# Optimization experiments

Measured on AMD Instinct MI355X. Metric: run time of the kernel, lower is better.

Reference implementation:

```python
import jax, jax.numpy as jnp
import numpy as np

LN_EPS = 1e-5

def _layer_norm(x, g, b):
    mu = jnp.mean(x, axis=-1, keepdims=True)
    var = jnp.var(x, axis=-1, keepdims=True)
    return (x - mu) * jax.lax.rsqrt(var + LN_EPS) * g + b

def _mlp(x, W1, b1, g1, beta1, W2, b2):
    h = x @ W1 + b1
    h = _layer_norm(h, g1, beta1)
    h = jax.nn.silu(h)
    return h @ W2 + b2

def setup_inputs() -> dict:
    key = jax.random.key(0)
    ks = jax.random.split(key, 16)
    N, E = 50000, 600000
    node_dim, edge_dim, hidden = 128, 128, 256
    def lin(k, fan_in, fan_out):
        bound = 1.0 / np.sqrt(fan_in)
        kw, kb = jax.random.split(k)
        W = jax.random.uniform(kw, (fan_in, fan_out), jnp.float32, -bound, bound)
        b = jax.random.uniform(kb, (fan_out,), jnp.float32, -bound, bound)
        return W, b
    eW1, eb1 = lin(ks[0], 2 * node_dim + edge_dim, hidden)
    eW2, eb2 = lin(ks[1], hidden, edge_dim)
    nW1, nb1 = lin(ks[2], node_dim + edge_dim, hidden)
    nW2, nb2 = lin(ks[3], hidden, node_dim)
    return {
        "node_features": jax.random.normal(ks[4], (N, node_dim), jnp.float32),
        "edge_features": jax.random.normal(ks[5], (E, edge_dim), jnp.float32),
        "edge_index": jax.random.randint(ks[6], (2, E), 0, N, jnp.int64),
        "eW1": eW1, "eb1": eb1, "eg1": jnp.ones((hidden,), jnp.float32), "ebeta1": jnp.zeros((hidden,), jnp.float32),
        "eW2": eW2, "eb2": eb2,
        "nW1": nW1, "nb1": nb1, "ng1": jnp.ones((hidden,), jnp.float32), "nbeta1": jnp.zeros((hidden,), jnp.float32),
        "nW2": nW2, "nb2": nb2,
    }

def reference(node_features, edge_features, edge_index,
              eW1, eb1, eg1, ebeta1, eW2, eb2,
              nW1, nb1, ng1, nbeta1, nW2, nb2):
    senders = edge_index[0]
    receivers = edge_index[1]
    # gather -> edge MLP (residual)
    edge_input = jnp.concatenate(
        [node_features[senders], node_features[receivers], edge_features], axis=-1)  # [E, 2*nd+ed]
    edge_features = edge_features + _mlp(edge_input, eW1, eb1, eg1, ebeta1, eW2, eb2)
    # scatter-add aggregate over receivers
    n_nodes = node_features.shape[0]
    aggregated = jax.ops.segment_sum(edge_features, receivers, num_segments=n_nodes)
    # node MLP (residual)
    node_input = jnp.concatenate([node_features, aggregated], axis=-1)  # [N, nd+ed]
    node_features = node_features + _mlp(node_input, nW1, nb1, ng1, nbeta1, nW2, nb2)
    return node_features, edge_features
```

## Files before the change

kernel.cpp:

```cpp
#include <hip/hip_runtime.h>

#define N_NODES 50000
#define N_EDGES 600000
#define DIM 128
#define HID 256
#define MR 32

typedef float  f32x4  __attribute__((ext_vector_type(4), aligned(16), may_alias));
typedef float  f32x2  __attribute__((ext_vector_type(2), aligned(8),  may_alias));
typedef __bf16 bf16x8 __attribute__((ext_vector_type(8), aligned(16), may_alias));
typedef int    i32x4  __attribute__((ext_vector_type(4), aligned(16), may_alias));

static __device__ inline f32x4 mfma16x16x32(bf16x8 a, bf16x8 b, f32x4 c) {
    return __builtin_amdgcn_mfma_f32_16x16x32_bf16(a, b, c, 0, 0, 0);
}

static __device__ inline bf16x8 cvt2_bf16(f32x4 a, f32x4 b) {
    bf16x8 o;
    o[0] = (__bf16)a[0]; o[1] = (__bf16)a[1]; o[2] = (__bf16)a[2]; o[3] = (__bf16)a[3];
    o[4] = (__bf16)b[0]; o[5] = (__bf16)b[1]; o[6] = (__bf16)b[2]; o[7] = (__bf16)b[3];
    return o;
}

__global__ void nbf_kernel(const float* __restrict__ node, __bf16* __restrict__ nbf) {
    int idx = blockIdx.x * 256 + threadIdx.x;
    if (idx >= N_NODES * 16) return;
    int row = idx >> 4, c = idx & 15;
    const float* p = node + (size_t)row * DIM + (c << 3);
    f32x4 a = ((const f32x4*)p)[0], b = ((const f32x4*)p)[1];
    *(bf16x8*)(nbf + (size_t)row * DIM + (c << 3)) = cvt2_bf16(a, b);
}

static __device__ inline void pack_one(const float* __restrict__ W,
                                       __bf16* __restrict__ out,
                                       int idx, int Ncols) {
    int lane = idx & 63;
    int tc = idx >> 6;
    int nC = Ncols >> 4;
    int c = tc % nC;
    int t = tc / nC;
    int col = (c << 4) + (lane & 15);
    int k0 = (t << 5) + ((lane >> 4) << 3);
    bf16x8 v;
#pragma unroll
    for (int j = 0; j < 8; ++j) v[j] = (__bf16)W[(k0 + j) * Ncols + col];
    *((bf16x8*)out + idx) = v;
}

__global__ void pack_all_kernel(const float* __restrict__ eW1, const float* __restrict__ eW2,
                                const float* __restrict__ nW1, const float* __restrict__ nW2,
                                __bf16* __restrict__ peW1, __bf16* __restrict__ peW2,
                                __bf16* __restrict__ pnW1, __bf16* __restrict__ pnW2) {
    int idx = blockIdx.x * 256 + threadIdx.x;
    if (idx < 12288)       pack_one(eW1, peW1, idx, 256);
    else if (idx < 16384)  pack_one(eW2, peW2, idx - 12288, 128);
    else if (idx < 24576)  pack_one(nW1, pnW1, idx - 16384, 256);
    else                   pack_one(nW2, pnW2, idx - 24576, 128);
}

__global__ void hist_kernel(const int* __restrict__ eidx, int* __restrict__ counts) {
    int e = blockIdx.x * 256 + threadIdx.x;
    if (e < N_EDGES) {
        int r = eidx[N_EDGES + e];
        r = (r < 0) ? 0 : (r >= N_NODES ? N_NODES - 1 : r);
        atomicAdd(&counts[r], 1);
    }
}

__global__ __launch_bounds__(1024) void scan_kernel(const int* __restrict__ counts,
                                                    int* __restrict__ offsets,
                                                    int* __restrict__ cursor) {
    __shared__ int part[1024];
    const int t = threadIdx.x;
    const int CH = (N_NODES + 1023) / 1024;
    const int base = t * CH;
    int s = 0;
#pragma unroll 1
    for (int i = 0; i < CH; ++i) {
        int idx = base + i;
        if (idx < N_NODES) s += counts[idx];
    }
    part[t] = s;
    __syncthreads();
    for (int d = 1; d < 1024; d <<= 1) {
        int x = (t >= d) ? part[t - d] : 0;
        __syncthreads();
        part[t] += x;
        __syncthreads();
    }
    int run = part[t] - s;
#pragma unroll 1
    for (int i = 0; i < CH; ++i) {
        int idx = base + i;
        if (idx < N_NODES) {
            offsets[idx] = run;
            cursor[idx]  = run;
            run += counts[idx];
        }
    }
    if (t == 1023) offsets[N_NODES] = run;
}

__global__ void scatter_kernel(const int* __restrict__ eidx,
                               int* __restrict__ cursor, int* __restrict__ eids) {
    int e = blockIdx.x * 256 + threadIdx.x;
    if (e < N_EDGES) {
        int r = eidx[N_EDGES + e];
        r = (r < 0) ? 0 : (r >= N_NODES ? N_NODES - 1 : r);
        int pos = atomicAdd(&cursor[r], 1);
        eids[pos] = e;
    }
}

template<int ASTRIDE, int T1>
__device__ inline void mlp_core(char* lds,
                                const bf16x8* __restrict__ pW1,
                                const bf16x8* __restrict__ pW2,
                                const float* __restrict__ b1,
                                const float* __restrict__ g1,
                                const float* __restrict__ be1,
                                f32x4 (&acc2)[2][2]) {
    const int tid = threadIdx.x;
    const int w = tid >> 6;
    const int lane = tid & 63;
    const int l16 = lane & 15;
    const int g = lane >> 4;
    float* stats = (float*)(lds + 32 * ASTRIDE);

    f32x4 acc[2][4];
#pragma unroll
    for (int m = 0; m < 2; ++m)
#pragma unroll
        for (int n = 0; n < 4; ++n) acc[m][n] = (f32x4){0.f, 0.f, 0.f, 0.f};
#pragma unroll
    for (int t = 0; t < T1; ++t) {
        bf16x8 af[2];
#pragma unroll
        for (int m = 0; m < 2; ++m)
            af[m] = *(const bf16x8*)(lds + (m * 16 + l16) * ASTRIDE + t * 64 + g * 16);
        const bf16x8* bp = pW1 + ((t * 16 + 4 * w) << 6) + lane;
#pragma unroll
        for (int n = 0; n < 4; ++n) {
            bf16x8 bf = bp[n << 6];
#pragma unroll
            for (int m = 0; m < 2; ++m)
                acc[m][n] = mfma16x16x32(af[m], bf, acc[m][n]);
        }
    }

    float b1v[4];
#pragma unroll
    for (int n = 0; n < 4; ++n) b1v[n] = b1[64 * w + 16 * n + l16];
#pragma unroll
    for (int m = 0; m < 2; ++m) {
#pragma unroll
        for (int n = 0; n < 4; ++n) acc[m][n] += b1v[n];
        f32x4 s = (acc[m][0] + acc[m][1]) + (acc[m][2] + acc[m][3]);
        f32x4 q = acc[m][0] * acc[m][0];
        q = acc[m][1] * acc[m][1] + q;
        q = acc[m][2] * acc[m][2] + q;
        q = acc[m][3] * acc[m][3] + q;
#pragma unroll
        for (int st = 1; st <= 8; st <<= 1) {
#pragma unroll
            for (int r = 0; r < 4; ++r) {
                s[r] += __shfl_xor(s[r], st);
                q[r] += __shfl_xor(q[r], st);
            }
        }
        if (l16 == 0) {
#pragma unroll
            for (int r = 0; r < 4; ++r) {
                int row = m * 16 + g * 4 + r;
                *(f32x2*)(stats + row * 8 + w * 2) = (f32x2){s[r], q[r]};
            }
        }
    }
    __syncthreads();

    f32x4 mu4[2], rs4[2];
#pragma unroll
    for (int m = 0; m < 2; ++m)
#pragma unroll
        for (int r = 0; r < 4; ++r) {
            int row = m * 16 + g * 4 + r;
            f32x4 a = *(const f32x4*)(stats + row * 8);
            f32x4 b = *(const f32x4*)(stats + row * 8 + 4);
            float S = (a[0] + a[2]) + (b[0] + b[2]);
            float Q = (a[1] + a[3]) + (b[1] + b[3]);
            float mm = S * (1.f / 256.f);
            float vv = fmaxf(Q * (1.f / 256.f) - mm * mm, 0.f);
            mu4[m][r] = mm;
            rs4[m][r] = __builtin_amdgcn_rsqf(vv + 1e-5f);
        }
    float g1v[4], bev[4];
#pragma unroll
    for (int n = 0; n < 4; ++n) {
        g1v[n] = g1[64 * w + 16 * n + l16];
        bev[n] = be1[64 * w + 16 * n + l16];
    }
#pragma unroll
    for (int m = 0; m < 2; ++m)
#pragma unroll
        for (int n = 0; n < 4; ++n) {
            f32x4 y = (acc[m][n] - mu4[m]) * rs4[m];
            y = y * g1v[n] + bev[n];
            int col = 64 * w + 16 * n + l16;
#pragma unroll
            for (int r = 0; r < 4; ++r) {
                float e = __builtin_amdgcn_exp2f(y[r] * -1.44269504f);
                float x = y[r] * __builtin_amdgcn_rcpf(1.f + e);
                int row = m * 16 + g * 4 + r;
                *(__bf16*)(lds + row * 528 + col * 2) = (__bf16)x;
            }
        }
    __syncthreads();

#pragma unroll
    for (int m = 0; m < 2; ++m)
#pragma unroll
        for (int n = 0; n < 2; ++n) acc2[m][n] = (f32x4){0.f, 0.f, 0.f, 0.f};
#pragma unroll
    for (int t = 0; t < 8; ++t) {
        bf16x8 af[2];
#pragma unroll
        for (int m = 0; m < 2; ++m)
            af[m] = *(const bf16x8*)(lds + (m * 16 + l16) * 528 + t * 64 + g * 16);
        const bf16x8* bp = pW2 + ((t * 8 + 2 * w) << 6) + lane;
#pragma unroll
        for (int n = 0; n < 2; ++n) {
            bf16x8 bf = bp[n << 6];
#pragma unroll
            for (int m = 0; m < 2; ++m)
                acc2[m][n] = mfma16x16x32(af[m], bf, acc2[m][n]);
        }
    }
}

__global__ __launch_bounds__(256, 5) void edge_kernel(
    const __bf16* __restrict__ nbf, const float* __restrict__ ef,
    const int* __restrict__ eidx,
    const bf16x8* __restrict__ pW1, const bf16x8* __restrict__ pW2,
    const float* __restrict__ b1, const float* __restrict__ g1,
    const float* __restrict__ be1, const float* __restrict__ b2,
    float* __restrict__ out_edges) {
    __shared__ __align__(16) char lds[MR * 784 + MR * 32];
    const int tid = threadIdx.x;
    const int eb = blockIdx.x * MR;

    {
        int row = tid >> 3, l8 = tid & 7;
        int e = eb + row;
        int snd = eidx[e], rcv = eidx[N_EDGES + e];
        snd = (snd < 0) ? 0 : (snd >= N_NODES ? N_NODES - 1 : snd);
        rcv = (rcv < 0) ? 0 : (rcv >= N_NODES ? N_NODES - 1 : rcv);
        const char* ps = (const char*)(nbf + (size_t)snd * DIM) + (l8 << 5);
        const char* pr = (const char*)(nbf + (size_t)rcv * DIM) + (l8 << 5);
        char* dst = lds + row * 784 + (l8 << 5);
        *(i32x4*)dst         = *(const i32x4*)ps;
        *(i32x4*)(dst + 16)  = *(const i32x4*)(ps + 16);
        *(i32x4*)(dst + 256) = *(const i32x4*)pr;
        *(i32x4*)(dst + 272) = *(const i32x4*)(pr + 16);
        const float* pe = ef + (size_t)e * DIM + (l8 << 4);
        f32x4 a0 = ((const f32x4*)pe)[0], a1 = ((const f32x4*)pe)[1];
        f32x4 a2 = ((const f32x4*)pe)[2], a3 = ((const f32x4*)pe)[3];
        *(bf16x8*)(dst + 512) = cvt2_bf16(a0, a1);
        *(bf16x8*)(dst + 528) = cvt2_bf16(a2, a3);
    }
    __syncthreads();

    f32x4 acc2[2][2];
    mlp_core<784, 12>(lds, pW1, pW2, b1, g1, be1, acc2);

    {
        const int w = tid >> 6, lane = tid & 63;
        const int l16 = lane & 15, g = lane >> 4;
        float b2v[2];
#pragma unroll
        for (int n = 0; n < 2; ++n) b2v[n] = b2[32 * w + 16 * n + l16];
#pragma unroll
        for (int m = 0; m < 2; ++m)
#pragma unroll
            for (int n = 0; n < 2; ++n)
#pragma unroll
                for (int r = 0; r < 4; ++r) {
                    int e = eb + m * 16 + g * 4 + r;
                    int col = 32 * w + 16 * n + l16;
                    size_t off = (size_t)e * DIM + col;
                    out_edges[off] = acc2[m][n][r] + b2v[n] + ef[off];
                }
    }
}

__global__ __launch_bounds__(256, 5) void node_kernel(
    const float* __restrict__ node, const __bf16* __restrict__ nbf,
    const float* __restrict__ out_edges,
    const int* __restrict__ offsets, const int* __restrict__ eids,
    const bf16x8* __restrict__ pW1, const bf16x8* __restrict__ pW2,
    const float* __restrict__ b1, const float* __restrict__ g1,
    const float* __restrict__ be1, const float* __restrict__ b2,
    float* __restrict__ out_nodes) {
    __shared__ __align__(16) char lds[MR * 528 + MR * 32];
    const int tid = threadIdx.x;
    const int nb = blockIdx.x * MR;

    {
        int row = tid >> 3, l8 = tid & 7;
        int n = nb + row;
        int nc = (n > N_NODES - 1) ? N_NODES - 1 : n;
        const char* pn = (const char*)(nbf + (size_t)nc * DIM) + (l8 << 5);
        char* dst = lds + row * 528 + (l8 << 5);
        *(i32x4*)dst        = *(const i32x4*)pn;
        *(i32x4*)(dst + 16) = *(const i32x4*)(pn + 16);
        float a[16];
#pragma unroll
        for (int j = 0; j < 16; ++j) a[j] = 0.f;
        int st = offsets[nc], en = offsets[nc + 1];
        int i = st;
#pragma unroll 1
        for (; i + 2 <= en; i += 2) {
            int e0 = eids[i], e1 = eids[i + 1];
            const float* er0 = out_edges + (size_t)e0 * DIM + (l8 << 4);
            const float* er1 = out_edges + (size_t)e1 * DIM + (l8 << 4);
            f32x4 u0 = ((const f32x4*)er0)[0], u1 = ((const f32x4*)er0)[1];
            f32x4 u2 = ((const f32x4*)er0)[2], u3 = ((const f32x4*)er0)[3];
            f32x4 v0 = ((const f32x4*)er1)[0], v1 = ((const f32x4*)er1)[1];
            f32x4 v2 = ((const f32x4*)er1)[2], v3 = ((const f32x4*)er1)[3];
#pragma unroll
            for (int k = 0; k < 4; ++k) {
                a[0 + k]  += u0[k] + v0[k];
                a[4 + k]  += u1[k] + v1[k];
                a[8 + k]  += u2[k] + v2[k];
                a[12 + k] += u3[k] + v3[k];
            }
        }
        if (i < en) {
            int e0 = eids[i];
            const float* er0 = out_edges + (size_t)e0 * DIM + (l8 << 4);
#pragma unroll
            for (int k = 0; k < 4; ++k) {
                f32x4 v = ((const f32x4*)er0)[k];
                a[k * 4 + 0] += v[0]; a[k * 4 + 1] += v[1];
                a[k * 4 + 2] += v[2]; a[k * 4 + 3] += v[3];
            }
        }
        bf16x8 o0, o1;
#pragma unroll
        for (int j = 0; j < 8; ++j) { o0[j] = (__bf16)a[j]; o1[j] = (__bf16)a[8 + j]; }
        int cbase = 16 + (l8 << 1);
        *(bf16x8*)(lds + row * 528 + (cbase << 4)) = o0;
        *(bf16x8*)(lds + row * 528 + ((cbase + 1) << 4)) = o1;
    }
    __syncthreads();

    f32x4 acc2[2][2];
    mlp_core<528, 8>(lds, pW1, pW2, b1, g1, be1, acc2);

    {
        const int w = tid >> 6, lane = tid & 63;
        const int l16 = lane & 15, g = lane >> 4;
        float b2v[2];
#pragma unroll
        for (int n = 0; n < 2; ++n) b2v[n] = b2[32 * w + 16 * n + l16];
#pragma unroll
        for (int m = 0; m < 2; ++m)
#pragma unroll
            for (int n = 0; n < 2; ++n)
#pragma unroll
                for (int r = 0; r < 4; ++r) {
                    int nd = nb + m * 16 + g * 4 + r;
                    if (nd < N_NODES) {
                        int col = 32 * w + 16 * n + l16;
                        size_t off = (size_t)nd * DIM + col;
                        out_nodes[off] = acc2[m][n][r] + b2v[n] + node[off];
                    }
                }
    }
}

extern "C" void kernel_launch(void* const* d_in, const int* in_sizes, int n_in,
                              void* d_out, int out_size, void* d_ws, size_t ws_size,
                              hipStream_t stream) {
    const float* node  = (const float*)d_in[0];
    const float* ef    = (const float*)d_in[1];
    const int*   eidx  = (const int*)d_in[2];
    const float* eW1   = (const float*)d_in[3];
    const float* eb1   = (const float*)d_in[4];
    const float* eg1   = (const float*)d_in[5];
    const float* ebt1  = (const float*)d_in[6];
    const float* eW2   = (const float*)d_in[7];
    const float* eb2   = (const float*)d_in[8];
    const float* nW1   = (const float*)d_in[9];
    const float* nb1   = (const float*)d_in[10];
    const float* ng1   = (const float*)d_in[11];
    const float* nbt1  = (const float*)d_in[12];
    const float* nW2   = (const float*)d_in[13];
    const float* nb2   = (const float*)d_in[14];

    char* ws = (char*)d_ws;
    int* counts  = (int*)ws;
    int* offsets = counts + 50016;
    int* cursor  = offsets + 50016;
    int* eids    = cursor + 50016;
    char* nbase = (char*)(eids + 600064);
    __bf16* nbf = (__bf16*)(((uintptr_t)nbase + 255) & ~(uintptr_t)255);
    __bf16* peW1 = nbf + (size_t)N_NODES * DIM;
    __bf16* peW2 = peW1 + 384 * 256;
    __bf16* pnW1 = peW2 + 256 * 128;
    __bf16* pnW2 = pnW1 + 256 * 256;

    hipMemsetAsync(counts, 0, 50000 * sizeof(int), stream);
    nbf_kernel<<<(N_NODES * 16 + 255) / 256, 256, 0, stream>>>(node, nbf);
    pack_all_kernel<<<112, 256, 0, stream>>>(eW1, eW2, nW1, nW2, peW1, peW2, pnW1, pnW2);

    hist_kernel<<<(N_EDGES + 255) / 256, 256, 0, stream>>>(eidx, counts);
    scan_kernel<<<1, 1024, 0, stream>>>(counts, offsets, cursor);
    scatter_kernel<<<(N_EDGES + 255) / 256, 256, 0, stream>>>(eidx, cursor, eids);

    float* out_nodes = (float*)d_out;
    float* out_edges = out_nodes + (size_t)N_NODES * DIM;

    edge_kernel<<<N_EDGES / MR, 256, 0, stream>>>(
        nbf, ef, eidx, (const bf16x8*)peW1, (const bf16x8*)peW2,
        eb1, eg1, ebt1, eb2, out_edges);
    node_kernel<<<(N_NODES + MR - 1) / MR, 256, 0, stream>>>(
        node, nbf, out_edges, offsets, eids, (const bf16x8*)pnW1, (const bf16x8*)pnW2,
        nb1, ng1, nbt1, nb2, out_nodes);
}
```

Before: 618.9 us.

## Double MLP row tile to 64 with 8-wave blocks and centralized LayerNorm stats

Raises rows per block from 32 to 64 and launches 512-thread blocks. Each wave now computes 4 row tiles by a narrower column slice, so every weight fragment loaded from global memory feeds twice as many MFMAs, roughly halving weight traffic per row. LayerNorm mean and rstd are now computed once per row by 64 threads and shared through LDS, instead of every lane recomputing them. The cost is a larger LDS footprint per block, which can lower the number of resident blocks per CU, and more accumulator registers per wave.

```diff
diff --git a/kernel.cpp b/kernel.cpp
--- a/kernel.cpp
+++ b/kernel.cpp
@@ -4,7 +4,7 @@
 #define N_EDGES 600000
 #define DIM 128
 #define HID 256
-#define MR 32
+#define MR 64
 
 typedef float  f32x4  __attribute__((ext_vector_type(4), aligned(16), may_alias));
 typedef float  f32x2  __attribute__((ext_vector_type(2), aligned(8),  may_alias));
@@ -113,53 +113,51 @@
 }
 
 template<int ASTRIDE, int T1>
-__device__ inline void mlp_core(char* lds,
-                                const bf16x8* __restrict__ pW1,
-                                const bf16x8* __restrict__ pW2,
-                                const float* __restrict__ b1,
-                                const float* __restrict__ g1,
-                                const float* __restrict__ be1,
-                                f32x4 (&acc2)[2][2]) {
+__device__ inline void mlp_core8(char* lds,
+                                 const bf16x8* __restrict__ pW1,
+                                 const bf16x8* __restrict__ pW2,
+                                 const float* __restrict__ b1,
+                                 const float* __restrict__ g1,
+                                 const float* __restrict__ be1,
+                                 f32x4 (&acc2)[4]) {
     const int tid = threadIdx.x;
     const int w = tid >> 6;
     const int lane = tid & 63;
     const int l16 = lane & 15;
     const int g = lane >> 4;
-    float* stats = (float*)(lds + 32 * ASTRIDE);
-
-    f32x4 acc[2][4];
-#pragma unroll
-    for (int m = 0; m < 2; ++m)
-#pragma unroll
-        for (int n = 0; n < 4; ++n) acc[m][n] = (f32x4){0.f, 0.f, 0.f, 0.f};
+    float* stats = (float*)(lds + 64 * ASTRIDE);
+
+    f32x4 acc[4][2];
+#pragma unroll
+    for (int m = 0; m < 4; ++m)
+#pragma unroll
+        for (int n = 0; n < 2; ++n) acc[m][n] = (f32x4){0.f, 0.f, 0.f, 0.f};
 #pragma unroll
     for (int t = 0; t < T1; ++t) {
-        bf16x8 af[2];
-#pragma unroll
-        for (int m = 0; m < 2; ++m)
+        bf16x8 af[4];
+#pragma unroll
+        for (int m = 0; m < 4; ++m)
             af[m] = *(const bf16x8*)(lds + (m * 16 + l16) * ASTRIDE + t * 64 + g * 16);
-        const bf16x8* bp = pW1 + ((t * 16 + 4 * w) << 6) + lane;
-#pragma unroll
-        for (int n = 0; n < 4; ++n) {
+        const bf16x8* bp = pW1 + ((t * 16 + 2 * w) << 6) + lane;
+#pragma unroll
+        for (int n = 0; n < 2; ++n) {
             bf16x8 bf = bp[n << 6];
 #pragma unroll
-            for (int m = 0; m < 2; ++m)
+            for (int m = 0; m < 4; ++m)
                 acc[m][n] = mfma16x16x32(af[m], bf, acc[m][n]);
         }
     }
 
-    float b1v[4];
-#pragma unroll
-    for (int n = 0; n < 4; ++n) b1v[n] = b1[64 * w + 16 * n + l16];
-#pragma unroll
-    for (int m = 0; m < 2; ++m) {
-#pragma unroll
-        for (int n = 0; n < 4; ++n) acc[m][n] += b1v[n];
-        f32x4 s = (acc[m][0] + acc[m][1]) + (acc[m][2] + acc[m][3]);
+    float b1v[2];
+#pragma unroll
+    for (int n = 0; n < 2; ++n) b1v[n] = b1[32 * w + 16 * n + l16];
+#pragma unroll
+    for (int m = 0; m < 4; ++m) {
+        acc[m][0] += b1v[0];
+        acc[m][1] += b1v[1];
+        f32x4 s = acc[m][0] + acc[m][1];
         f32x4 q = acc[m][0] * acc[m][0];
         q = acc[m][1] * acc[m][1] + q;
-        q = acc[m][2] * acc[m][2] + q;
-        q = acc[m][3] * acc[m][3] + q;
 #pragma unroll
         for (int st = 1; st <= 8; st <<= 1) {
 #pragma unroll
@@ -172,40 +170,46 @@
 #pragma unroll
             for (int r = 0; r < 4; ++r) {
                 int row = m * 16 + g * 4 + r;
-                *(f32x2*)(stats + row * 8 + w * 2) = (f32x2){s[r], q[r]};
-            }
-        }
-    }
-    __syncthreads();
-
-    f32x4 mu4[2], rs4[2];
-#pragma unroll
-    for (int m = 0; m < 2; ++m)
+                *(f32x2*)(stats + row * 16 + w * 2) = (f32x2){s[r], q[r]};
+            }
+        }
+    }
+    __syncthreads();
+
+    if (tid < 64) {
+        const float* sp = stats + tid * 16;
+        f32x4 a = *(const f32x4*)sp;
+        f32x4 b = *(const f32x4*)(sp + 4);
+        f32x4 c = *(const f32x4*)(sp + 8);
+        f32x4 d = *(const f32x4*)(sp + 12);
+        float S = ((a[0] + a[2]) + (b[0] + b[2])) + ((c[0] + c[2]) + (d[0] + d[2]));
+        float Q = ((a[1] + a[3]) + (b[1] + b[3])) + ((c[1] + c[3]) + (d[1] + d[3]));
+        float mm = S * (1.f / 256.f);
+        float vv = fmaxf(Q * (1.f / 256.f) - mm * mm, 0.f);
+        *(f32x2*)(stats + tid * 16) = (f32x2){mm, __builtin_amdgcn_rsqf(vv + 1e-5f)};
+    }
+    __syncthreads();
+
+    float g1v[2], bev[2];
+#pragma unroll
+    for (int n = 0; n < 2; ++n) {
+        g1v[n] = g1[32 * w + 16 * n + l16];
+        bev[n] = be1[32 * w + 16 * n + l16];
+    }
+#pragma unroll
+    for (int m = 0; m < 4; ++m) {
+        f32x4 mu4, rs4;
 #pragma unroll
         for (int r = 0; r < 4; ++r) {
             int row = m * 16 + g * 4 + r;
-            f32x4 a = *(const f32x4*)(stats + row * 8);
-            f32x4 b = *(const f32x4*)(stats + row * 8 + 4);
-            float S = (a[0] + a[2]) + (b[0] + b[2]);
-            float Q = (a[1] + a[3]) + (b[1] + b[3]);
-            float mm = S * (1.f / 256.f);
-            float vv = fmaxf(Q * (1.f / 256.f) - mm * mm, 0.f);
-            mu4[m][r] = mm;
-            rs4[m][r] = __builtin_amdgcn_rsqf(vv + 1e-5f);
-        }
-    float g1v[4], bev[4];
-#pragma unroll
-    for (int n = 0; n < 4; ++n) {
-        g1v[n] = g1[64 * w + 16 * n + l16];
-        bev[n] = be1[64 * w + 16 * n + l16];
-    }
-#pragma unroll
-    for (int m = 0; m < 2; ++m)
-#pragma unroll
-        for (int n = 0; n < 4; ++n) {
-            f32x4 y = (acc[m][n] - mu4[m]) * rs4[m];
+            f32x2 v = *(const f32x2*)(stats + row * 16);
+            mu4[r] = v[0]; rs4[r] = v[1];
+        }
+#pragma unroll
+        for (int n = 0; n < 2; ++n) {
+            f32x4 y = (acc[m][n] - mu4) * rs4;
             y = y * g1v[n] + bev[n];
-            int col = 64 * w + 16 * n + l16;
+            int col = 32 * w + 16 * n + l16;
 #pragma unroll
             for (int r = 0; r < 4; ++r) {
                 float e = __builtin_amdgcn_exp2f(y[r] * -1.44269504f);
@@ -214,37 +218,32 @@
                 *(__bf16*)(lds + row * 528 + col * 2) = (__bf16)x;
             }
         }
-    __syncthreads();
-
-#pragma unroll
-    for (int m = 0; m < 2; ++m)
-#pragma unroll
-        for (int n = 0; n < 2; ++n) acc2[m][n] = (f32x4){0.f, 0.f, 0.f, 0.f};
+    }
+    __syncthreads();
+
+#pragma unroll
+    for (int m = 0; m < 4; ++m) acc2[m] = (f32x4){0.f, 0.f, 0.f, 0.f};
 #pragma unroll
     for (int t = 0; t < 8; ++t) {
-        bf16x8 af[2];
-#pragma unroll
-        for (int m = 0; m < 2; ++m)
+        bf16x8 af[4];
+#pragma unroll
+        for (int m = 0; m < 4; ++m)
             af[m] = *(const bf16x8*)(lds + (m * 16 + l16) * 528 + t * 64 + g * 16);
-        const bf16x8* bp = pW2 + ((t * 8 + 2 * w) << 6) + lane;
-#pragma unroll
-        for (int n = 0; n < 2; ++n) {
-            bf16x8 bf = bp[n << 6];
-#pragma unroll
-            for (int m = 0; m < 2; ++m)
-                acc2[m][n] = mfma16x16x32(af[m], bf, acc2[m][n]);
-        }
-    }
-}
-
-__global__ __launch_bounds__(256, 5) void edge_kernel(
+        bf16x8 bf = pW2[((t * 8 + w) << 6) + lane];
+#pragma unroll
+        for (int m = 0; m < 4; ++m)
+            acc2[m] = mfma16x16x32(af[m], bf, acc2[m]);
+    }
+}
+
+__global__ __launch_bounds__(512, 6) void edge_kernel(
     const __bf16* __restrict__ nbf, const float* __restrict__ ef,
     const int* __restrict__ eidx,
     const bf16x8* __restrict__ pW1, const bf16x8* __restrict__ pW2,
     const float* __restrict__ b1, const float* __restrict__ g1,
     const float* __restrict__ be1, const float* __restrict__ b2,
     float* __restrict__ out_edges) {
-    __shared__ __align__(16) char lds[MR * 784 + MR * 32];
+    __shared__ __align__(16) char lds[MR * 784 + MR * 64];
     const int tid = threadIdx.x;
     const int eb = blockIdx.x * MR;
 
@@ -269,30 +268,26 @@
     }
     __syncthreads();
 
-    f32x4 acc2[2][2];
-    mlp_core<784, 12>(lds, pW1, pW2, b1, g1, be1, acc2);
+    f32x4 acc2[4];
+    mlp_core8<784, 12>(lds, pW1, pW2, b1, g1, be1, acc2);
 
     {
         const int w = tid >> 6, lane = tid & 63;
         const int l16 = lane & 15, g = lane >> 4;
-        float b2v[2];
-#pragma unroll
-        for (int n = 0; n < 2; ++n) b2v[n] = b2[32 * w + 16 * n + l16];
-#pragma unroll
-        for (int m = 0; m < 2; ++m)
-#pragma unroll
-            for (int n = 0; n < 2; ++n)
-#pragma unroll
-                for (int r = 0; r < 4; ++r) {
-                    int e = eb + m * 16 + g * 4 + r;
-                    int col = 32 * w + 16 * n + l16;
-                    size_t off = (size_t)e * DIM + col;
-                    out_edges[off] = acc2[m][n][r] + b2v[n] + ef[off];
-                }
-    }
-}
-
-__global__ __launch_bounds__(256, 5) void node_kernel(
+        const int col = 16 * w + l16;
+        float b2v = b2[col];
+#pragma unroll
+        for (int m = 0; m < 4; ++m)
+#pragma unroll
+            for (int r = 0; r < 4; ++r) {
+                int e = eb + m * 16 + g * 4 + r;
+                size_t off = (size_t)e * DIM + col;
+                out_edges[off] = acc2[m][r] + b2v + ef[off];
+            }
+    }
+}
+
+__global__ __launch_bounds__(512, 6) void node_kernel(
     const float* __restrict__ node, const __bf16* __restrict__ nbf,
     const float* __restrict__ out_edges,
     const int* __restrict__ offsets, const int* __restrict__ eids,
@@ -300,7 +295,7 @@
     const float* __restrict__ b1, const float* __restrict__ g1,
     const float* __restrict__ be1, const float* __restrict__ b2,
     float* __restrict__ out_nodes) {
-    __shared__ __align__(16) char lds[MR * 528 + MR * 32];
+    __shared__ __align__(16) char lds[MR * 528 + MR * 64];
     const int tid = threadIdx.x;
     const int nb = blockIdx.x * MR;
 
@@ -353,28 +348,24 @@
     }
     __syncthreads();
 
-    f32x4 acc2[2][2];
-    mlp_core<528, 8>(lds, pW1, pW2, b1, g1, be1, acc2);
+    f32x4 acc2[4];
+    mlp_core8<528, 8>(lds, pW1, pW2, b1, g1, be1, acc2);
 
     {
         const int w = tid >> 6, lane = tid & 63;
         const int l16 = lane & 15, g = lane >> 4;
-        float b2v[2];
-#pragma unroll
-        for (int n = 0; n < 2; ++n) b2v[n] = b2[32 * w + 16 * n + l16];
-#pragma unroll
-        for (int m = 0; m < 2; ++m)
-#pragma unroll
-            for (int n = 0; n < 2; ++n)
-#pragma unroll
-                for (int r = 0; r < 4; ++r) {
-                    int nd = nb + m * 16 + g * 4 + r;
-                    if (nd < N_NODES) {
-                        int col = 32 * w + 16 * n + l16;
-                        size_t off = (size_t)nd * DIM + col;
-                        out_nodes[off] = acc2[m][n][r] + b2v[n] + node[off];
-                    }
+        const int col = 16 * w + l16;
+        float b2v = b2[col];
+#pragma unroll
+        for (int m = 0; m < 4; ++m)
+#pragma unroll
+            for (int r = 0; r < 4; ++r) {
+                int nd = nb + m * 16 + g * 4 + r;
+                if (nd < N_NODES) {
+                    size_t off = (size_t)nd * DIM + col;
+                    out_nodes[off] = acc2[m][r] + b2v + node[off];
                 }
+            }
     }
 }
 
@@ -420,10 +411,10 @@
     float* out_nodes = (float*)d_out;
     float* out_edges = out_nodes + (size_t)N_NODES * DIM;
 
-    edge_kernel<<<N_EDGES / MR, 256, 0, stream>>>(
+    edge_kernel<<<N_EDGES / MR, 512, 0, stream>>>(
         nbf, ef, eidx, (const bf16x8*)peW1, (const bf16x8*)peW2,
         eb1, eg1, ebt1, eb2, out_edges);
-    node_kernel<<<(N_NODES + MR - 1) / MR, 256, 0, stream>>>(
+    node_kernel<<<(N_NODES + MR - 1) / MR, 512, 0, stream>>>(
         node, nbf, out_edges, offsets, eids, (const bf16x8*)pnW1, (const bf16x8*)pnW2,
         nb1, ng1, nbt1, nb2, out_nodes);
 }
```

Measured after the change: 736.3 us. 1.19x slower.
